# Performance work log

Hardware: AMD Instinct MI355X
Metric: run time of the kernel (lower is better)

## Reference

```python
import jax, jax.numpy as jnp
import numpy as np

B = 32768
K = 4096  # num_embeddings
D = 512   # embedding_dim
COMMITMENT_COST = 0.25


def setup_inputs() -> dict:
    key = jax.random.key(0)
    k1, k2 = jax.random.split(key)
    inputs = jax.random.normal(k1, (B, D), dtype=jnp.float32)
    # nn.Embedding weight init: uniform(-1/K, 1/K)
    codebook = jax.random.uniform(k2, (K, D), dtype=jnp.float32,
                                  minval=-1.0 / K, maxval=1.0 / K)
    return {"inputs": inputs, "codebook": codebook}


def reference(inputs, codebook):
    distances = (jnp.sum(inputs ** 2, axis=1, keepdims=True)
                 + jnp.sum(codebook ** 2, axis=1)
                 - 2.0 * jnp.matmul(inputs, codebook.T))
    encoding_indices = jnp.argmin(distances, axis=1)  # [B]
    # one-hot encodings are part of the module's returned dict
    encodings = jax.nn.one_hot(encoding_indices, K, dtype=inputs.dtype)  # [B, K]
    # quantized = encodings @ codebook == direct gather (same math)
    quantized = codebook[encoding_indices]  # [B, D]

    sg = jax.lax.stop_gradient
    e_latent_loss = jnp.mean((sg(quantized) - inputs) ** 2)
    q_latent_loss = jnp.mean((quantized - sg(inputs)) ** 2)
    loss = q_latent_loss + COMMITMENT_COST * e_latent_loss

    # straight-through estimator
    quantized_st = inputs + sg(quantized - inputs)

    avg_probs = jnp.mean(encodings, axis=0)  # [K]
    perplexity = jnp.exp(-jnp.sum(avg_probs * jnp.log(avg_probs + 1e-10)))

    return quantized_st, encoding_indices, loss, perplexity, encodings
```

## Files before the change

kernel.cpp:

```cpp
#include <hip/hip_runtime.h>
#include <hip/hip_bf16.h>


typedef __attribute__((ext_vector_type(8))) short bf16x8;
typedef __attribute__((ext_vector_type(4))) float f32x4;

#define BB 32768
#define KK 4096
#define DD 512

#define IDX_OFF  (BB*DD)
#define LOSS_OFF (IDX_OFF + BB)
#define PERP_OFF (LOSS_OFF + 1)
#define ENC_OFF  (PERP_OFF + 1)

#define WSB_XSQ  0
#define WSB_ESQ  131072
#define WSB_IDX  147456
#define WSB_HIST 278528
#define WSB_LOSS 294912
#define WSB_EBF2 294928
#define WSB_XBF  4489232
#define WSB_PART 38043664

#define MARG 2.5e-4f
#define NCAND 16

static __device__ __forceinline__ unsigned short f2bf(float f) {
    __hip_bfloat16 h = __float2bfloat16(f);
    return *reinterpret_cast<unsigned short*>(&h);
}

static __device__ __forceinline__ unsigned int packscore(float s, int col) {
    unsigned int u = __float_as_uint(s);
    u ^= (u & 0x80000000u) ? 0xFFFFFFFFu : 0x80000000u;
    return (u & 0xFFFFF000u) | (unsigned int)col;
}
static __device__ __forceinline__ float unpackscore(unsigned int p) {
    unsigned int u = p & 0xFFFFF000u;
    u = (u & 0x80000000u) ? (u ^ 0x80000000u) : ~u;
    return __uint_as_float(u);
}

static __device__ __forceinline__ void gll16(const void* g, void* l) {
    __builtin_amdgcn_global_load_lds(
        (const __attribute__((address_space(1))) unsigned int*)g,
        (__attribute__((address_space(3))) unsigned int*)l, 16, 0, 0);
}

__global__ __launch_bounds__(256) void init_kernel(int* __restrict__ hist,
                                                   double* __restrict__ loss_acc) {
    int i = blockIdx.x * 256 + threadIdx.x;
    if (i < KK) hist[i] = 0;
    if (i == 0) *loss_acc = 0.0;
}

__global__ __launch_bounds__(256) void npsum_pack_kernel(const float* __restrict__ X,
                                                         const float* __restrict__ E,
                                                         float* __restrict__ xsq,
                                                         float* __restrict__ esq,
                                                         unsigned short* __restrict__ Xbf) {
    __shared__ float sq[4][512];
    __shared__ float ub[4][64];
    __shared__ float bb[4][4];
    int w = threadIdx.x >> 6, lane = threadIdx.x & 63;
    int row = blockIdx.x * 4 + w;
    const float* src; float* dst;
    bool isx = (row < BB);
    if (isx) { src = X + (size_t)row * DD;        dst = xsq + row; }
    else     { src = E + (size_t)(row - BB) * DD; dst = esq + (row - BB); }
    const float4* s4 = (const float4*)(src + lane * 8);
    float4 a = s4[0], b = s4[1];
    sq[w][lane * 8 + 0] = __fmul_rn(a.x, a.x);
    sq[w][lane * 8 + 1] = __fmul_rn(a.y, a.y);
    sq[w][lane * 8 + 2] = __fmul_rn(a.z, a.z);
    sq[w][lane * 8 + 3] = __fmul_rn(a.w, a.w);
    sq[w][lane * 8 + 4] = __fmul_rn(b.x, b.x);
    sq[w][lane * 8 + 5] = __fmul_rn(b.y, b.y);
    sq[w][lane * 8 + 6] = __fmul_rn(b.z, b.z);
    sq[w][lane * 8 + 7] = __fmul_rn(b.w, b.w);
    if (isx) {
        int kt64 = lane >> 3, ks = (lane >> 2) & 1, oct = lane & 3;
        int rf = (row >> 4) & 15;
        size_t unit = ((size_t)((row >> 8) * 8 + kt64)) * 2048
                    + (size_t)((rf * 2 + ks) * 64 + oct * 16 + (row & 15));
        union { bf16x8 v; unsigned short us[8]; } pk;
        pk.us[0] = f2bf(a.x); pk.us[1] = f2bf(a.y); pk.us[2] = f2bf(a.z); pk.us[3] = f2bf(a.w);
        pk.us[4] = f2bf(b.x); pk.us[5] = f2bf(b.y); pk.us[6] = f2bf(b.z); pk.us[7] = f2bf(b.w);
        *(bf16x8*)(Xbf + unit * 8) = pk.v;
    }
    __syncthreads();
    {
        int b2 = lane >> 4, l = lane & 15;
        const float* s = &sq[w][b2 * 128];
        float t = __fadd_rn(
            __fadd_rn(__fadd_rn(s[l], s[16 + l]), __fadd_rn(s[32 + l], s[48 + l])),
            __fadd_rn(__fadd_rn(s[64 + l], s[80 + l]), __fadd_rn(s[96 + l], s[112 + l])));
        ub[w][lane] = t;
    }
    __syncthreads();
    if (lane < 4) {
        const float* u = &ub[w][lane * 16];
        float T3[8], T6[4];
        #pragma unroll
        for (int i = 0; i < 8; ++i) T3[i] = __fadd_rn(u[i], u[i + 8]);
        #pragma unroll
        for (int i = 0; i < 4; ++i) T6[i] = __fadd_rn(T3[i], T3[i + 4]);
        bb[w][lane] = __fadd_rn(__fadd_rn(T6[0], T6[2]), __fadd_rn(T6[1], T6[3]));
    }
    __syncthreads();
    if (lane == 0)
        *dst = __fadd_rn(__fadd_rn(bb[w][0], bb[w][1]), __fadd_rn(bb[w][2], bb[w][3]));
}

__global__ __launch_bounds__(256) void packE_kernel(const float* __restrict__ src,
                                                    unsigned short* __restrict__ dst) {
    int t = blockIdx.x * 256 + threadIdx.x;
    int chunk = t >> 11, u = t & 2047;
    int rb2 = chunk >> 3, kt = chunk & 7;
    int rf = u >> 7, ks = (u >> 6) & 1, lane = u & 63;
    int row = rb2 * 256 + rf * 16 + (lane & 15);
    int k   = kt * 64 + ks * 32 + (lane >> 4) * 8;
    const float4* s = (const float4*)(src + (size_t)row * DD + k);
    float4 a = s[0], b = s[1];
    union { bf16x8 v; unsigned short us[8]; } pk;
    pk.us[0] = f2bf(a.x); pk.us[1] = f2bf(a.y); pk.us[2] = f2bf(a.z); pk.us[3] = f2bf(a.w);
    pk.us[4] = f2bf(b.x); pk.us[5] = f2bf(b.y); pk.us[6] = f2bf(b.z); pk.us[7] = f2bf(b.w);
    *(bf16x8*)(dst + (size_t)t * 8) = pk.v;
}

__global__ __launch_bounds__(256, 4) void gemm_screen(
    const unsigned short* __restrict__ Xbf, const unsigned short* __restrict__ Ebf2,
    const float* __restrict__ esqw, uint2* __restrict__ partials)
{
    __shared__ __align__(16) char pool[32768];

    const int tid = threadIdx.x;
    const int w = tid >> 6, lane = tid & 63;
    const int c = lane & 15, g = lane >> 4;
    const int bid = blockIdx.x;
    const int orig = (bid & 7) * 1024 + (bid >> 3);
    const int rb = orig >> 5, cb = orig & 31;
    const int row0 = rb * 128, col0 = cb * 128;
    const int mw = w >> 1, nw = w & 1;

    const int hA = rb & 1, hB = cb & 1;
    const char* Xc = (const char*)Xbf  + (size_t)(rb >> 1) * 8 * 32768;
    const char* Ec = (const char*)Ebf2 + (size_t)(cb >> 1) * 8 * 32768;

    f32x4 acc[4][4];
    #pragma unroll
    for (int i = 0; i < 4; ++i)
        #pragma unroll
        for (int j = 0; j < 4; ++j) acc[i][j] = (f32x4){0.f, 0.f, 0.f, 0.f};

    #define STAGE(srcc_, h_, kt_, dstoff_) { \
        const char* sb_ = (srcc_) + (size_t)((kt_) >> 1) * 32768; \
        const int ks_ = (kt_) & 1; \
        _Pragma("unroll") for (int it_ = 0; it_ < 2; ++it_) { \
            const char* s_ = sb_ + (size_t)((((h_) * 8 + it_ * 4 + w) * 2 + ks_) * 64 + lane) * 16; \
            char* d_ = pool + (dstoff_) + (it_ * 4 + w) * 1024; \
            gll16(s_, d_); } }

    STAGE(Xc, hA, 0, 0); STAGE(Ec, hB, 0, 16384);
    int buf = 0;
    for (int kt = 0; kt < 16; ++kt) {
        if (kt < 15) {
            STAGE(Xc, hA, kt + 1, (buf ^ 1) * 8192);
            STAGE(Ec, hB, kt + 1, 16384 + (buf ^ 1) * 8192);
            asm volatile("s_waitcnt vmcnt(4)" ::: "memory");
        } else {
            asm volatile("s_waitcnt vmcnt(0)" ::: "memory");
        }
        __builtin_amdgcn_s_barrier();
        const char* Ap = pool + buf * 8192;
        const char* Bp = pool + 16384 + buf * 8192;
        bf16x8 af[4], bfr[4];
        #pragma unroll
        for (int i = 0; i < 4; ++i) {
            af[i]  = *(const bf16x8*)(Ap + (((mw * 4 + i) * 64) + lane) * 16);
            bfr[i] = *(const bf16x8*)(Bp + (((nw * 4 + i) * 64) + lane) * 16);
        }
        __builtin_amdgcn_s_setprio(1);
        #pragma unroll
        for (int mf = 0; mf < 4; ++mf)
            #pragma unroll
            for (int nf = 0; nf < 4; ++nf)
                acc[mf][nf] = __builtin_amdgcn_mfma_f32_16x16x32_bf16(af[mf], bfr[nf], acc[mf][nf], 0, 0, 0);
        __builtin_amdgcn_s_setprio(0);
        __builtin_amdgcn_s_barrier();
        buf ^= 1;
    }

    uint2* P = (uint2*)pool;
    #pragma unroll
    for (int mf = 0; mf < 4; ++mf) {
        #pragma unroll
        for (int r = 0; r < 4; ++r) {
            unsigned int q1 = 0xFFFFFFFFu, q2 = 0xFFFFFFFFu;
            int rowl = mw * 64 + mf * 16 + g * 4 + r;
            #pragma unroll
            for (int nf = 0; nf < 4; ++nf) {
                int col = col0 + nw * 64 + nf * 16 + c;
                float s = fmaf(-2.0f, acc[mf][nf][r], esqw[col]);
                unsigned int q = packscore(s, col);
                if (q < q1) { q2 = q1; q1 = q; } else if (q < q2) q2 = q;
            }
            P[(nw * 128 + rowl) * 16 + c] = make_uint2(q1, q2);
        }
    }
    __syncthreads();
    if (tid < 128) {
        int row = tid;
        #pragma unroll
        for (int n2 = 0; n2 < 2; ++n2) {
            unsigned int m1 = 0xFFFFFFFFu, m2 = 0xFFFFFFFFu;
            #pragma unroll 4
            for (int cc = 0; cc < 16; ++cc) {
                uint2 e = P[(n2 * 128 + row) * 16 + cc];
                if (e.x < m1) { m2 = m1; m1 = e.x; } else if (e.x < m2) m2 = e.x;
                if (e.y < m1) { m2 = m1; m1 = e.y; } else if (e.y < m2) m2 = e.y;
            }
            partials[(size_t)(cb * 2 + n2) * BB + row0 + row] = make_uint2(m1, m2);
        }
    }
    #undef STAGE
}

__global__ __launch_bounds__(256) void reduce_kernel(
    const float* __restrict__ X, const float* __restrict__ E,
    const float* __restrict__ xsqw, const float* __restrict__ esqw,
    const uint2* __restrict__ partials, int* __restrict__ idxbuf,
    int* __restrict__ hist, double* __restrict__ loss_acc,
    float* __restrict__ out)
{
    __shared__ double lred[256];
    const int row = blockIdx.x * 256 + threadIdx.x;
    unsigned int m = 0xFFFFFFFFu;
    for (int e = 0; e < 64; ++e) m = min(m, partials[(size_t)e * BB + row].x);
    float lim = unpackscore(m) + MARG;
    int cand[NCAND]; int nc = 0;
    for (int e = 0; e < 64; ++e) {
        uint2 p = partials[(size_t)e * BB + row];
        if (unpackscore(p.x) <= lim && nc < NCAND) cand[nc++] = (int)(p.x & 0xFFFu);
        if (unpackscore(p.y) <= lim && nc < NCAND) cand[nc++] = (int)(p.y & 0xFFFu);
    }
    const float* xr = X + (size_t)row * DD;
    float xs = xsqw[row];
    float bd = 3.0e38f; int bk = 0x7fffffff;
    for (int cidx = 0; cidx < nc; ++cidx) {
        int k = cand[cidx] & (KK - 1);
        const float* er = E + (size_t)k * DD;
        float q1 = 0.f, q2 = 0.f;
        for (int d = 0; d < 384; ++d)   q1 = fmaf(xr[d], er[d], q1);
        for (int d = 384; d < 512; ++d) q2 = fmaf(xr[d], er[d], q2);
        float dot = __fadd_rn(q1, q2);
        float t1  = __fadd_rn(xs, esqw[k]);
        float dnp = __fsub_rn(t1, __fmul_rn(2.0f, dot));
        if (dnp < bd || (dnp == bd && k < bk)) { bd = dnp; bk = k; }
    }
    const float* er = E + (size_t)bk * DD;
    double ls = 0.0;
    for (int d = 0; d < DD; ++d) {
        double df = (double)xr[d] - (double)er[d];
        ls = fma(df, df, ls);
    }
    idxbuf[row] = bk;
    out[IDX_OFF + row] = (float)bk;
    atomicAdd(&hist[bk], 1);
    lred[threadIdx.x] = ls;
    __syncthreads();
    for (int t = 128; t > 0; t >>= 1) {
        if (threadIdx.x < t) lred[threadIdx.x] += lred[threadIdx.x + t];
        __syncthreads();
    }
    if (threadIdx.x == 0) atomicAdd(loss_acc, lred[0]);
}

__global__ __launch_bounds__(256) void encq_kernel(const int* __restrict__ idxbuf,
                                                   const float* __restrict__ E,
                                                   float* __restrict__ out) {
    int row = blockIdx.x;
    int idx = idxbuf[row];
    ((float2*)out)[(size_t)row * 256 + threadIdx.x] =
        ((const float2*)E)[(size_t)idx * 256 + threadIdx.x];
    float2* erow = (float2*)(out + ENC_OFF) + (size_t)row * (KK / 2);
    int half = idx >> 1;
    float2 one;
    if (idx & 1) { one.x = 0.f; one.y = 1.f; } else { one.x = 1.f; one.y = 0.f; }
    float2 z; z.x = 0.f; z.y = 0.f;
    for (int cc = threadIdx.x; cc < KK / 2; cc += 256)
        erow[cc] = (cc == half) ? one : z;
}

__global__ __launch_bounds__(256) void fin_kernel(const int* __restrict__ hist,
                                                  const double* __restrict__ loss_acc,
                                                  float* __restrict__ out) {
    __shared__ double red[256];
    int tid = threadIdx.x;
    double s = 0.0;
    for (int k = tid; k < KK; k += 256) {
        double p = (double)hist[k] * (1.0 / 32768.0);
        s += p * log(p + 1e-10);
    }
    red[tid] = s;
    __syncthreads();
    for (int t = 128; t > 0; t >>= 1) {
        if (tid < t) red[tid] += red[tid + t];
        __syncthreads();
    }
    if (tid == 0) {
        double perp = exp(-red[0]);
        double L = loss_acc[0] * (1.0 / ((double)BB * (double)DD));
        out[LOSS_OFF] = (float)(1.25 * L);
        out[PERP_OFF] = (float)perp;
    }
}

extern "C" void kernel_launch(void* const* d_in, const int* in_sizes, int n_in,
                              void* d_out, int out_size, void* d_ws, size_t ws_size,
                              hipStream_t stream) {
    const float* X; const float* E;
    if (in_sizes[0] == BB * DD) { X = (const float*)d_in[0]; E = (const float*)d_in[1]; }
    else                        { X = (const float*)d_in[1]; E = (const float*)d_in[0]; }
    float* out = (float*)d_out;

    float* xsq = (float*)((char*)d_ws + WSB_XSQ);
    float* esq = (float*)((char*)d_ws + WSB_ESQ);
    int* idxbuf = (int*)((char*)d_ws + WSB_IDX);
    int* hist   = (int*)((char*)d_ws + WSB_HIST);
    double* loss_acc = (double*)((char*)d_ws + WSB_LOSS);
    unsigned short* Ebf2 = (unsigned short*)((char*)d_ws + WSB_EBF2);
    unsigned short* Xbf  = (unsigned short*)((char*)d_ws + WSB_XBF);
    uint2* partials = (uint2*)((char*)d_ws + WSB_PART);

    hipLaunchKernelGGL(init_kernel, dim3(16), dim3(256), 0, stream, hist, loss_acc);
    hipLaunchKernelGGL(npsum_pack_kernel, dim3((BB + KK) / 4), dim3(256), 0, stream,
                       X, E, xsq, esq, Xbf);
    hipLaunchKernelGGL(packE_kernel, dim3(1024), dim3(256), 0, stream, E, Ebf2);
    hipLaunchKernelGGL(gemm_screen, dim3(8192), dim3(256), 0, stream,
                       Xbf, Ebf2, esq, partials);
    hipLaunchKernelGGL(reduce_kernel, dim3(BB / 256), dim3(256), 0, stream,
                       X, E, xsq, esq, partials, idxbuf, hist, loss_acc, out);
    hipLaunchKernelGGL(encq_kernel, dim3(BB), dim3(256), 0, stream, idxbuf, E, out);
    hipLaunchKernelGGL(fin_kernel, dim3(1), dim3(256), 0, stream, hist, loss_acc, out);
}
```

Before: 453.1 us.

## Fuse candidate rescoring with gather and one-hot write; fold init into packE

Merges the reduce kernel and the encodings/quantized write kernel into one finalize kernel. Each block of 256 threads rescores 32 rows using only 32 threads, then all 256 threads write the gathered codebook rows and the one-hot rows. The init kernel is folded into packE, which removes two launches and the index buffer round trip. The cost is that only 32 of 256 threads do the serial candidate rescoring, so the latency-bound rescoring phase has far lower parallelism per block, and the wide stores cannot start until it finishes.

```diff
diff --git a/kernel.cpp b/kernel.cpp
--- a/kernel.cpp
+++ b/kernel.cpp
@@ -16,7 +16,6 @@
 
 #define WSB_XSQ  0
 #define WSB_ESQ  131072
-#define WSB_IDX  147456
 #define WSB_HIST 278528
 #define WSB_LOSS 294912
 #define WSB_EBF2 294928
@@ -46,13 +45,6 @@
     __builtin_amdgcn_global_load_lds(
         (const __attribute__((address_space(1))) unsigned int*)g,
         (__attribute__((address_space(3))) unsigned int*)l, 16, 0, 0);
-}
-
-__global__ __launch_bounds__(256) void init_kernel(int* __restrict__ hist,
-                                                   double* __restrict__ loss_acc) {
-    int i = blockIdx.x * 256 + threadIdx.x;
-    if (i < KK) hist[i] = 0;
-    if (i == 0) *loss_acc = 0.0;
 }
 
 __global__ __launch_bounds__(256) void npsum_pack_kernel(const float* __restrict__ X,
@@ -114,8 +106,12 @@
 }
 
 __global__ __launch_bounds__(256) void packE_kernel(const float* __restrict__ src,
-                                                    unsigned short* __restrict__ dst) {
+                                                    unsigned short* __restrict__ dst,
+                                                    int* __restrict__ hist,
+                                                    double* __restrict__ loss_acc) {
     int t = blockIdx.x * 256 + threadIdx.x;
+    if (t < KK) hist[t] = 0;
+    if (t == KK) *loss_acc = 0.0;
     int chunk = t >> 11, u = t & 2047;
     int rb2 = chunk >> 3, kt = chunk & 7;
     int rf = u >> 7, ks = (u >> 6) & 1, lane = u & 63;
@@ -227,70 +223,79 @@
     #undef STAGE
 }
 
-__global__ __launch_bounds__(256) void reduce_kernel(
+__global__ __launch_bounds__(256) void finalize_kernel(
     const float* __restrict__ X, const float* __restrict__ E,
     const float* __restrict__ xsqw, const float* __restrict__ esqw,
-    const uint2* __restrict__ partials, int* __restrict__ idxbuf,
-    int* __restrict__ hist, double* __restrict__ loss_acc,
-    float* __restrict__ out)
+    const uint2* __restrict__ partials, int* __restrict__ hist,
+    double* __restrict__ loss_acc, float* __restrict__ out)
 {
-    __shared__ double lred[256];
-    const int row = blockIdx.x * 256 + threadIdx.x;
-    unsigned int m = 0xFFFFFFFFu;
-    for (int e = 0; e < 64; ++e) m = min(m, partials[(size_t)e * BB + row].x);
-    float lim = unpackscore(m) + MARG;
-    int cand[NCAND]; int nc = 0;
-    for (int e = 0; e < 64; ++e) {
-        uint2 p = partials[(size_t)e * BB + row];
-        if (unpackscore(p.x) <= lim && nc < NCAND) cand[nc++] = (int)(p.x & 0xFFFu);
-        if (unpackscore(p.y) <= lim && nc < NCAND) cand[nc++] = (int)(p.y & 0xFFFu);
-    }
-    const float* xr = X + (size_t)row * DD;
-    float xs = xsqw[row];
-    float bd = 3.0e38f; int bk = 0x7fffffff;
-    for (int cidx = 0; cidx < nc; ++cidx) {
-        int k = cand[cidx] & (KK - 1);
-        const float* er = E + (size_t)k * DD;
-        float q1 = 0.f, q2 = 0.f;
-        for (int d = 0; d < 384; ++d)   q1 = fmaf(xr[d], er[d], q1);
-        for (int d = 384; d < 512; ++d) q2 = fmaf(xr[d], er[d], q2);
-        float dot = __fadd_rn(q1, q2);
-        float t1  = __fadd_rn(xs, esqw[k]);
-        float dnp = __fsub_rn(t1, __fmul_rn(2.0f, dot));
-        if (dnp < bd || (dnp == bd && k < bk)) { bd = dnp; bk = k; }
-    }
-    const float* er = E + (size_t)bk * DD;
-    double ls = 0.0;
-    for (int d = 0; d < DD; ++d) {
-        double df = (double)xr[d] - (double)er[d];
-        ls = fma(df, df, ls);
-    }
-    idxbuf[row] = bk;
-    out[IDX_OFF + row] = (float)bk;
-    atomicAdd(&hist[bk], 1);
-    lred[threadIdx.x] = ls;
-    __syncthreads();
-    for (int t = 128; t > 0; t >>= 1) {
-        if (threadIdx.x < t) lred[threadIdx.x] += lred[threadIdx.x + t];
-        __syncthreads();
-    }
-    if (threadIdx.x == 0) atomicAdd(loss_acc, lred[0]);
-}
-
-__global__ __launch_bounds__(256) void encq_kernel(const int* __restrict__ idxbuf,
-                                                   const float* __restrict__ E,
-                                                   float* __restrict__ out) {
-    int row = blockIdx.x;
-    int idx = idxbuf[row];
-    ((float2*)out)[(size_t)row * 256 + threadIdx.x] =
-        ((const float2*)E)[(size_t)idx * 256 + threadIdx.x];
-    float2* erow = (float2*)(out + ENC_OFF) + (size_t)row * (KK / 2);
-    int half = idx >> 1;
-    float2 one;
-    if (idx & 1) { one.x = 0.f; one.y = 1.f; } else { one.x = 1.f; one.y = 0.f; }
-    float2 z; z.x = 0.f; z.y = 0.f;
-    for (int cc = threadIdx.x; cc < KK / 2; cc += 256)
-        erow[cc] = (cc == half) ? one : z;
+    __shared__ int sidx[32];
+    __shared__ double lsr[32];
+    const int tid = threadIdx.x;
+    const int row0 = blockIdx.x * 32;
+
+    if (tid < 32) {
+        const int row = row0 + tid;
+        unsigned int m = 0xFFFFFFFFu;
+        for (int e = 0; e < 64; ++e) m = min(m, partials[(size_t)e * BB + row].x);
+        float lim = unpackscore(m) + MARG;
+        int cand[NCAND]; int nc = 0;
+        for (int e = 0; e < 64; ++e) {
+            uint2 p = partials[(size_t)e * BB + row];
+            if (unpackscore(p.x) <= lim && nc < NCAND) cand[nc++] = (int)(p.x & 0xFFFu);
+            if (unpackscore(p.y) <= lim && nc < NCAND) cand[nc++] = (int)(p.y & 0xFFFu);
+        }
+        const float* xr = X + (size_t)row * DD;
+        float xs = xsqw[row];
+        float bd = 3.0e38f; int bk = 0x7fffffff;
+        for (int cidx = 0; cidx < nc; ++cidx) {
+            int k = cand[cidx] & (KK - 1);
+            const float* er = E + (size_t)k * DD;
+            float q1 = 0.f, q2 = 0.f;
+            for (int d = 0; d < 384; ++d)   q1 = fmaf(xr[d], er[d], q1);
+            for (int d = 384; d < 512; ++d) q2 = fmaf(xr[d], er[d], q2);
+            float dot = __fadd_rn(q1, q2);
+            float t1  = __fadd_rn(xs, esqw[k]);
+            float dnp = __fsub_rn(t1, __fmul_rn(2.0f, dot));
+            if (dnp < bd || (dnp == bd && k < bk)) { bd = dnp; bk = k; }
+        }
+        const float* er = E + (size_t)bk * DD;
+        double ls = 0.0;
+        for (int d = 0; d < DD; ++d) {
+            double df = (double)xr[d] - (double)er[d];
+            ls = fma(df, df, ls);
+        }
+        sidx[tid] = bk;
+        lsr[tid] = ls;
+        out[IDX_OFF + row] = (float)bk;
+        atomicAdd(&hist[bk], 1);
+    }
+    __syncthreads();
+    if (tid == 0) {
+        double s = 0.0;
+        #pragma unroll 8
+        for (int i = 0; i < 32; ++i) s += lsr[i];
+        atomicAdd(loss_acc, s);
+    }
+    #pragma unroll 4
+    for (int r = 0; r < 32; ++r) {
+        int idx = sidx[r];
+        ((float2*)out)[(size_t)(row0 + r) * 256 + tid] =
+            ((const float2*)E)[(size_t)idx * 256 + tid];
+    }
+    for (int r = 0; r < 32; ++r) {
+        int idx = sidx[r];
+        float2* erow = (float2*)(out + ENC_OFF) + (size_t)(row0 + r) * (KK / 2);
+        int half = idx >> 1;
+        float2 one;
+        if (idx & 1) { one.x = 0.f; one.y = 1.f; } else { one.x = 1.f; one.y = 0.f; }
+        float2 z; z.x = 0.f; z.y = 0.f;
+        #pragma unroll
+        for (int j = 0; j < 8; ++j) {
+            int cc = tid + j * 256;
+            erow[cc] = (cc == half) ? one : z;
+        }
+    }
 }
 
 __global__ __launch_bounds__(256) void fin_kernel(const int* __restrict__ hist,
@@ -327,21 +332,19 @@
 
     float* xsq = (float*)((char*)d_ws + WSB_XSQ);
     float* esq = (float*)((char*)d_ws + WSB_ESQ);
-    int* idxbuf = (int*)((char*)d_ws + WSB_IDX);
     int* hist   = (int*)((char*)d_ws + WSB_HIST);
     double* loss_acc = (double*)((char*)d_ws + WSB_LOSS);
     unsigned short* Ebf2 = (unsigned short*)((char*)d_ws + WSB_EBF2);
     unsigned short* Xbf  = (unsigned short*)((char*)d_ws + WSB_XBF);
     uint2* partials = (uint2*)((char*)d_ws + WSB_PART);
 
-    hipLaunchKernelGGL(init_kernel, dim3(16), dim3(256), 0, stream, hist, loss_acc);
     hipLaunchKernelGGL(npsum_pack_kernel, dim3((BB + KK) / 4), dim3(256), 0, stream,
                        X, E, xsq, esq, Xbf);
-    hipLaunchKernelGGL(packE_kernel, dim3(1024), dim3(256), 0, stream, E, Ebf2);
+    hipLaunchKernelGGL(packE_kernel, dim3(1024), dim3(256), 0, stream,
+                       E, Ebf2, hist, loss_acc);
     hipLaunchKernelGGL(gemm_screen, dim3(8192), dim3(256), 0, stream,
                        Xbf, Ebf2, esq, partials);
-    hipLaunchKernelGGL(reduce_kernel, dim3(BB / 256), dim3(256), 0, stream,
-                       X, E, xsq, esq, partials, idxbuf, hist, loss_acc, out);
-    hipLaunchKernelGGL(encq_kernel, dim3(BB), dim3(256), 0, stream, idxbuf, E, out);
+    hipLaunchKernelGGL(finalize_kernel, dim3(BB / 32), dim3(256), 0, stream,
+                       X, E, xsq, esq, partials, hist, loss_acc, out);
     hipLaunchKernelGGL(fin_kernel, dim3(1), dim3(256), 0, stream, hist, loss_acc, out);
 }
```

New measurement: 444.4 us. About the same (-1.9%).
